# Kernel tuning notes

Hardware: AMD Instinct MI355X
Metric: run time of the kernel (lower is better)

Reference implementation:

```python
import jax, jax.numpy as jnp
import numpy as np

UPDATE_STEPS = 2
EPS = 1e-7


def _collect(attn, source, W, b):
    """_Collection_Unit: relu(Linear(source)) gathered by attention, row-averaged.
    attn: [N_tgt, N_src], source: [N_src, D_in], W: [D_out, D_in], b: [D_out]."""
    fc_out = jax.nn.relu(source @ W.T + b)          # [N_src, D_out]
    collect = attn @ fc_out                          # [N_tgt, D_out]
    denom = jnp.sum(attn, axis=1, keepdims=True) + EPS
    return collect / denom


def setup_inputs() -> dict:
    key = jax.random.key(0)
    ks = jax.random.split(key, 10)
    N_OBJ, N_REL, D = 2048, 16384, 1024
    inp = {
        "obj_feats": jax.random.normal(ks[0], (N_OBJ, D), jnp.float32),
        "rel_feats": jax.random.normal(ks[1], (N_REL, D), jnp.float32),
        "attn_sub": jax.random.uniform(ks[2], (N_OBJ, N_REL), jnp.float32),
        "attn_obj": jax.random.uniform(ks[3], (N_OBJ, N_REL), jnp.float32),
        "attn_self": jax.random.uniform(ks[4], (N_OBJ, N_OBJ), jnp.float32),
    }
    # normal_init(fc, 0, 0.01) per original module
    names = ["rel2obj_sub", "rel2obj_obj", "obj2rel_sub", "obj2rel_obj", "obj2obj"]
    for i, n in enumerate(names):
        inp[f"W_{n}"] = jax.random.normal(ks[5 + i], (D, D), jnp.float32) * 0.01
        inp[f"b_{n}"] = jnp.zeros((D,), jnp.float32)
    return inp


def reference(obj_feats, rel_feats, attn_sub, attn_obj, attn_self,
              W_rel2obj_sub, b_rel2obj_sub, W_rel2obj_obj, b_rel2obj_obj,
              W_obj2rel_sub, b_obj2rel_sub, W_obj2rel_obj, b_obj2rel_obj,
              W_obj2obj, b_obj2obj):
    x_obj, x_rel = obj_feats, rel_feats
    for _ in range(UPDATE_STEPS):
        # collect to objects: from relations (as subject / as object) and from other objects
        src_sub = _collect(attn_sub, x_rel, W_rel2obj_sub, b_rel2obj_sub)   # unit 0
        src_obj = _collect(attn_obj, x_rel, W_rel2obj_obj, b_rel2obj_obj)   # unit 1
        src_self = _collect(attn_self, x_obj, W_obj2obj, b_obj2obj)         # unit 4
        src2obj = (src_sub + src_obj + src_self) / 3.0
        x_obj_new = x_obj + src2obj                                          # _Update_Unit 0
        # collect to relations: from subject / object node features
        src_rel_sub = _collect(attn_sub.T, x_obj, W_obj2rel_sub, b_obj2rel_sub)  # unit 2
        src_rel_obj = _collect(attn_obj.T, x_obj, W_obj2rel_obj, b_obj2rel_obj)  # unit 3
        src2rel = (src_rel_sub + src_rel_obj) / 2.0
        x_rel = x_rel + src2rel                                              # _Update_Unit 1
        x_obj = x_obj_new
    return x_obj, x_rel
```

## Files before the change

kernel.cpp:

```cpp
#include <hip/hip_runtime.h>
#include <hip/hip_bf16.h>

typedef __attribute__((ext_vector_type(4))) float  f32x4;
typedef __attribute__((ext_vector_type(8))) __bf16 bf16x8;
typedef __attribute__((ext_vector_type(4))) int    i32x4;
typedef __attribute__((ext_vector_type(8))) int    i32x8;
typedef __hip_bfloat16 bf16_t;

#define GT 256
#define BM 128
#define BN 128
#define BK 32

#define NOBJ 2048
#define NREL 16384
#define DIM  1024
#define KOBJ 34816
#define KREL 4096

#define AS1Q __attribute__((address_space(1)))
#define AS3Q __attribute__((address_space(3)))

__device__ __forceinline__ void gload_lds16(const void* g, void* l) {
    __builtin_amdgcn_global_load_lds((AS1Q void*)const_cast<void*>(g),
                                     (AS3Q void*)l, 16, 0, 0);
}

#define MFMA_BF16 __builtin_amdgcn_mfma_f32_16x16x32_bf16
#define MFMA_F8(ACC, Af, Bf) \
    ACC = __builtin_amdgcn_mfma_scale_f32_16x16x128_f8f6f4( \
        Af, Bf, ACC, 0, 0, 0, 0x7F7F7F7F, 0, 0x7F7F7F7F)

#define VMCNT(N) asm volatile("s_waitcnt vmcnt(" #N ")" ::: "memory")
#define SBAR()   __builtin_amdgcn_sched_barrier(0)

__device__ __forceinline__ unsigned char fp8_byte(float x) {
    return (unsigned char)(__builtin_amdgcn_cvt_pk_fp8_f32(x, x, 0, false) & 0xFF);
}
__device__ __forceinline__ unsigned pk4_fp8(float a, float b, float c, float d) {
    int v = __builtin_amdgcn_cvt_pk_fp8_f32(a, b, 0, false);
    v = __builtin_amdgcn_cvt_pk_fp8_f32(c, d, v, true);
    return (unsigned)v;
}

__global__ __launch_bounds__(GT)
void gemm_bt_f234(const bf16_t* __restrict__ A, const bf16_t* __restrict__ B,
                  int M, int N, int K, const float* __restrict__ vecM,
                  unsigned char* __restrict__ fcRel8, unsigned char* __restrict__ fcObj8)
{
    __shared__ bf16_t sA[BM * BK];
    __shared__ bf16_t sB[BN * BK];

    const int tid  = threadIdx.x;
    const int lane = tid & 63;
    const int wid  = tid >> 6;
    const int wr = wid >> 1, wc = wid & 1;
    const int l15 = lane & 15, lk = lane >> 4;

    const long rowA0 = (long)blockIdx.x * BM;
    const long rowB0 = (long)blockIdx.y * BN;
    const long ldab  = (long)K * 2;

    const int c0 = tid, c1 = tid + GT;
    const int r0c = c0 >> 2, k0c = (c0 & 3) ^ ((r0c >> 1) & 3);
    const int r1c = c1 >> 2, k1c = (c1 & 3) ^ ((r1c >> 1) & 3);

    const char* gA0 = (const char*)A + (rowA0 + r0c) * ldab + k0c * 16;
    const char* gA1 = (const char*)A + (rowA0 + r1c) * ldab + k1c * 16;
    const char* gB0 = (const char*)B + (rowB0 + r0c) * ldab + k0c * 16;
    const char* gB1 = (const char*)B + (rowB0 + r1c) * ldab + k1c * 16;
    char* lA0 = (char*)sA + c0 * 16;
    char* lA1 = (char*)sA + c1 * 16;
    char* lB0 = (char*)sB + c0 * 16;
    char* lB1 = (char*)sB + c1 * 16;

    f32x4 acc[4][4];
    #pragma unroll
    for (int i = 0; i < 4; i++)
        #pragma unroll
        for (int j = 0; j < 4; j++) acc[i][j] = f32x4{0.f, 0.f, 0.f, 0.f};

    const int ktPer = K / BK;
    for (int kt = 0; kt < ktPer; ++kt) {
        const long kByte = (long)kt * (BK * 2);
        gload_lds16(gA0 + kByte, lA0);
        gload_lds16(gA1 + kByte, lA1);
        gload_lds16(gB0 + kByte, lB0);
        gload_lds16(gB1 + kByte, lB1);
        __syncthreads();

        bf16x8 af[4], bg[4];
        #pragma unroll
        for (int i = 0; i < 4; i++) {
            const int rr = wr * 64 + i * 16 + l15;
            const int kk = lk ^ ((rr >> 1) & 3);
            af[i] = *reinterpret_cast<const bf16x8*>((const char*)sA + rr * 64 + kk * 16);
        }
        #pragma unroll
        for (int j = 0; j < 4; j++) {
            const int rr = wc * 64 + j * 16 + l15;
            const int kk = lk ^ ((rr >> 1) & 3);
            bg[j] = *reinterpret_cast<const bf16x8*>((const char*)sB + rr * 64 + kk * 16);
        }
        #pragma unroll
        for (int i = 0; i < 4; i++)
            #pragma unroll
            for (int j = 0; j < 4; j++)
                acc[i][j] = MFMA_BF16(af[i], bg[j], acc[i][j], 0, 0, 0);
        __syncthreads();
    }

    #pragma unroll
    for (int i = 0; i < 4; i++) {
        const long mBase = rowA0 + wr * 64 + i * 16 + lk * 4;
        const f32x4 vm = *reinterpret_cast<const f32x4*>(&vecM[mBase]);
        #pragma unroll
        for (int r = 0; r < 4; r++) {
            const long m = mBase + r;
            #pragma unroll
            for (int j = 0; j < 4; j++) {
                const long n = rowB0 + wc * 64 + j * 16 + l15;
                const float v = fmaxf(acc[i][j][r] + vm[r], 0.f);
                const unsigned char o = fp8_byte(v);
                if (m < 1024)            fcRel8[m * (long)KREL + n] = o;
                else if (m < 2048)       fcRel8[(m - 1024) * (long)KREL + 2048 + n] = o;
                else                     fcObj8[(m - 2048) * (long)KOBJ + 32768 + n] = o;
            }
        }
    }
}

__global__ __launch_bounds__(512, 2)
void gemm256fc(const bf16_t* __restrict__ A, const bf16_t* __restrict__ B,
               int M, int N, int K, const float* __restrict__ vecM,
               unsigned char* __restrict__ Cb8, int ldc, int Ntiles)
{
    __shared__ __align__(16) char lds[131072];

    const int tid  = threadIdx.x;
    const int lane = tid & 63;
    const int wid  = tid >> 6;
    const int wr = wid >> 2, wc = wid & 3;
    const int l15 = lane & 15, lk = lane >> 4;

    const int nwg = gridDim.x;
    const int cpx = nwg >> 3;
    const int bid = blockIdx.x;
    const int swz = (bid & 7) * cpx + (bid >> 3);
    const int tm = swz / Ntiles, tn = swz % Ntiles;
    const long rowM0 = (long)tm * 256;
    const long rowN0 = (long)tn * 256;
    const long ld = (long)K * 2;

    const int NT = K >> 6;

    const int rl = tid >> 3;
    const int lc = (tid & 7) ^ (rl & 7);
    const char* gA0 = (const char*)A + (rowM0 + rl) * ld + lc * 16;
    const char* gB0 = (const char*)B + (rowN0 + rl) * ld + lc * 16;

    auto stage = [&](int buf, int isB, int h, int t) {
        const char* g = (isB ? gB0 : gA0) + (long)h * 128 * ld + (long)t * 128;
        char* l = (char*)lds + buf * 65536 + isB * 32768 + h * 16384 + tid * 16;
        gload_lds16(g, l);
        gload_lds16(g + 64 * ld, l + 8192);
    };

    const int xo0 = ((0 + lk) ^ (l15 & 7)) * 16;
    const int xo1 = ((4 + lk) ^ (l15 & 7)) * 16;
    const int baseA = (wr * 16 + l15) * 128;
    const int baseB = 32768 + (wc * 16 + l15) * 128;

    f32x4 acc[8][4];
    #pragma unroll
    for (int i = 0; i < 8; i++)
        #pragma unroll
        for (int j = 0; j < 4; j++) acc[i][j] = f32x4{0.f, 0.f, 0.f, 0.f};

    stage(0, 0, 0, 0); stage(0, 1, 0, 0); stage(0, 1, 1, 0); stage(0, 0, 1, 0);

    bf16x8 a[4][2], b[4][2];
    for (int t = 0; t < NT; ++t) {
        const int cur = t & 1;
        const int nxt = cur ^ 1;
        const bool pf = (t + 1) < NT;
        const char* lcur = (const char*)lds + (cur << 16);

        if (pf) { stage(nxt, 0, 0, t + 1); stage(nxt, 1, 0, t + 1);
                  stage(nxt, 1, 1, t + 1); stage(nxt, 0, 1, t + 1); }
        if (pf) { VMCNT(10); } else { VMCNT(2); }
        SBAR();
        __builtin_amdgcn_s_barrier();

        #pragma unroll
        for (int kf = 0; kf < 4; kf++) {
            a[kf][0] = *(const bf16x8*)(lcur + baseA + kf * 4096 + xo0);
            a[kf][1] = *(const bf16x8*)(lcur + baseA + kf * 4096 + xo1);
        }
        #pragma unroll
        for (int j = 0; j < 4; j++) {
            b[j][0] = *(const bf16x8*)(lcur + baseB + j * 8192 + xo0);
            b[j][1] = *(const bf16x8*)(lcur + baseB + j * 8192 + xo1);
        }
        asm volatile("s_waitcnt lgkmcnt(0)" ::: "memory");
        SBAR();
        __builtin_amdgcn_s_setprio(1);
        #pragma unroll
        for (int j = 0; j < 4; j++)
            #pragma unroll
            for (int kf = 0; kf < 4; kf++) {
                acc[kf][j] = MFMA_BF16(a[kf][0], b[j][0], acc[kf][j], 0, 0, 0);
                acc[kf][j] = MFMA_BF16(a[kf][1], b[j][1], acc[kf][j], 0, 0, 0);
            }
        __builtin_amdgcn_s_setprio(0);
        if (pf) { VMCNT(8); } else { VMCNT(0); }
        SBAR();
        __builtin_amdgcn_s_barrier();

        #pragma unroll
        for (int kf = 0; kf < 4; kf++) {
            a[kf][0] = *(const bf16x8*)(lcur + baseA + (4 + kf) * 4096 + xo0);
            a[kf][1] = *(const bf16x8*)(lcur + baseA + (4 + kf) * 4096 + xo1);
        }
        asm volatile("s_waitcnt lgkmcnt(0)" ::: "memory");
        SBAR();
        __builtin_amdgcn_s_barrier();
        __builtin_amdgcn_s_setprio(1);
        #pragma unroll
        for (int j = 0; j < 4; j++)
            #pragma unroll
            for (int kf = 0; kf < 4; kf++) {
                acc[4 + kf][j] = MFMA_BF16(a[kf][0], b[j][0], acc[4 + kf][j], 0, 0, 0);
                acc[4 + kf][j] = MFMA_BF16(a[kf][1], b[j][1], acc[4 + kf][j], 0, 0, 0);
            }
        __builtin_amdgcn_s_setprio(0);
    }

    #pragma unroll
    for (int kf = 0; kf < 8; kf++) {
        const long m0 = rowM0 + wr * 16 + kf * 32 + lk * 4;
        const f32x4 vm = *reinterpret_cast<const f32x4*>(vecM + m0);
        #pragma unroll
        for (int r = 0; r < 4; r++) {
            const long m = m0 + r;
            #pragma unroll
            for (int j = 0; j < 4; j++) {
                const long n = rowN0 + wc * 16 + j * 64 + l15;
                const float o = fmaxf(acc[kf][j][r] + vm[r], 0.f);
                Cb8[(m & 1023) * (long)ldc + (m >> 10) * 16384 + n] = fp8_byte(o);
            }
        }
    }
}

__global__ __launch_bounds__(512, 2)
void gemm256f8(const unsigned char* __restrict__ A, const unsigned char* __restrict__ B,
               int M, int N, int K, float* __restrict__ Cf, float scale,
               int ldc, int Ntiles)
{
    __shared__ __align__(16) char lds[131072];

    const int tid  = threadIdx.x;
    const int lane = tid & 63;
    const int wid  = tid >> 6;
    const int wr = wid >> 2, wc = wid & 3;
    const int l15 = lane & 15, lk = lane >> 4;

    const int nwg = gridDim.x;
    const int cpx = nwg >> 3;
    const int bid = blockIdx.x;
    const int swz = (bid & 7) * cpx + (bid >> 3);
    const int tm = swz / Ntiles, tn = swz % Ntiles;
    const long rowM0 = (long)tm * 256;
    const long rowN0 = (long)tn * 256;
    const long ld = (long)K;

    const int nz = gridDim.z;
    const int NT = (K >> 7) / nz;
    const long kb0 = (long)NT * blockIdx.z * 128;

    const int rl = tid >> 3;
    const int lc = (tid & 7) ^ (rl & 7);
    const char* gA0 = (const char*)A + (rowM0 + rl) * ld + kb0 + lc * 16;
    const char* gB0 = (const char*)B + (rowN0 + rl) * ld + kb0 + lc * 16;

    auto stage = [&](int buf, int isB, int h, int t) {
        const char* g = (isB ? gB0 : gA0) + (long)h * 128 * ld + (long)t * 128;
        char* l = (char*)lds + buf * 65536 + isB * 32768 + h * 16384 + tid * 16;
        gload_lds16(g, l);
        gload_lds16(g + 64 * ld, l + 8192);
    };

    const int xc0 = ((2 * lk + 0) ^ (l15 & 7)) * 16;
    const int xc1 = ((2 * lk + 1) ^ (l15 & 7)) * 16;
    const int baseA = (wr * 16 + l15) * 128;
    const int baseB = 32768 + (wc * 16 + l15) * 128;

#define LDF8(dst, off) { \
    i32x4 lo_ = *(const i32x4*)(lcur + (off) + xc0); \
    i32x4 hi_ = *(const i32x4*)(lcur + (off) + xc1); \
    dst = __builtin_shufflevector(lo_, hi_, 0, 1, 2, 3, 4, 5, 6, 7); }

    f32x4 acc[8][4];
    #pragma unroll
    for (int i = 0; i < 8; i++)
        #pragma unroll
        for (int j = 0; j < 4; j++) acc[i][j] = f32x4{0.f, 0.f, 0.f, 0.f};

    stage(0, 0, 0, 0); stage(0, 1, 0, 0); stage(0, 1, 1, 0); stage(0, 0, 1, 0);

    i32x8 a[4], b[4];
    for (int t = 0; t < NT; ++t) {
        const int cur = t & 1;
        const int nxt = cur ^ 1;
        const bool pf = (t + 1) < NT;
        const char* lcur = (const char*)lds + (cur << 16);

        if (pf) { stage(nxt, 0, 0, t + 1); stage(nxt, 1, 0, t + 1);
                  stage(nxt, 1, 1, t + 1); stage(nxt, 0, 1, t + 1); }
        if (pf) { VMCNT(10); } else { VMCNT(2); }
        SBAR();
        __builtin_amdgcn_s_barrier();

        #pragma unroll
        for (int kf = 0; kf < 4; kf++) LDF8(a[kf], baseA + kf * 4096);
        #pragma unroll
        for (int j = 0; j < 4; j++)    LDF8(b[j], baseB + j * 8192);
        asm volatile("s_waitcnt lgkmcnt(0)" ::: "memory");
        SBAR();
        __builtin_amdgcn_s_setprio(1);
        #pragma unroll
        for (int j = 0; j < 4; j++)
            #pragma unroll
            for (int kf = 0; kf < 4; kf++) MFMA_F8(acc[kf][j], a[kf], b[j]);
        __builtin_amdgcn_s_setprio(0);
        if (pf) { VMCNT(8); } else { VMCNT(0); }
        SBAR();
        __builtin_amdgcn_s_barrier();

        #pragma unroll
        for (int kf = 0; kf < 4; kf++) LDF8(a[kf], baseA + (4 + kf) * 4096);
        asm volatile("s_waitcnt lgkmcnt(0)" ::: "memory");
        SBAR();
        __builtin_amdgcn_s_barrier();
        __builtin_amdgcn_s_setprio(1);
        #pragma unroll
        for (int j = 0; j < 4; j++)
            #pragma unroll
            for (int kf = 0; kf < 4; kf++) MFMA_F8(acc[4 + kf][j], a[kf], b[j]);
        __builtin_amdgcn_s_setprio(0);
    }
#undef LDF8

    #pragma unroll
    for (int kf = 0; kf < 8; kf++) {
        const long m0 = rowM0 + wr * 16 + kf * 32 + lk * 4;
        #pragma unroll
        for (int r = 0; r < 4; r++) {
            const long m = m0 + r;
            #pragma unroll
            for (int j = 0; j < 4; j++) {
                const long n = rowN0 + wc * 16 + j * 64 + l15;
                const float v = acc[kf][j][r] * scale;
                if (nz == 1) Cf[m * (long)ldc + n] += v;
                else atomicAdd(&Cf[m * (long)ldc + n], v);
            }
        }
    }
}

__global__ __launch_bounds__(256)
void k_cast_bf16(const float* __restrict__ in, bf16_t* __restrict__ out, long n)
{
    const long stride = (long)gridDim.x * blockDim.x;
    for (long i = (long)blockIdx.x * blockDim.x + threadIdx.x; i * 4 < n; i += stride) {
        f32x4 v = *reinterpret_cast<const f32x4*>(in + i * 4);
        union { bf16_t h[4]; ushort4 u; } o;
        o.h[0] = __float2bfloat16(v[0]); o.h[1] = __float2bfloat16(v[1]);
        o.h[2] = __float2bfloat16(v[2]); o.h[3] = __float2bfloat16(v[3]);
        *reinterpret_cast<ushort4*>(out + i * 4) = o.u;
    }
}

template<bool COLS>
__global__ __launch_bounds__(256)
void k_sums(const float* __restrict__ in, int C,
            float* __restrict__ rowsum, float* __restrict__ colsum)
{
    __shared__ float cpart[16][64];
    __shared__ float rpart[64][17];
    const int tid = threadIdx.x;
    const int tx  = tid & 15;
    const int ty  = tid >> 4;
    const long c0 = (long)blockIdx.x * 64;
    const long r0 = (long)blockIdx.y * 64;

    float cs0 = 0.f, cs1 = 0.f, cs2 = 0.f, cs3 = 0.f;
    #pragma unroll
    for (int i = 0; i < 4; i++) {
        const int r = i * 16 + ty;
        const f32x4 v = *reinterpret_cast<const f32x4*>(&in[(r0 + r) * (long)C + c0 + tx * 4]);
        rpart[r][tx] = v[0] + v[1] + v[2] + v[3];
        cs0 += v[0]; cs1 += v[1]; cs2 += v[2]; cs3 += v[3];
    }
    if (COLS) {
        cpart[ty][tx * 4 + 0] = cs0;
        cpart[ty][tx * 4 + 1] = cs1;
        cpart[ty][tx * 4 + 2] = cs2;
        cpart[ty][tx * 4 + 3] = cs3;
    }
    __syncthreads();
    if (tid < 64) {
        float rs = 0.f;
        #pragma unroll
        for (int k = 0; k < 16; k++) rs += rpart[tid][k];
        atomicAdd(&rowsum[r0 + tid], rs);
        if (COLS) {
            float cs = 0.f;
            #pragma unroll
            for (int k = 0; k < 16; k++) cs += cpart[k][tid];
            atomicAdd(&colsum[c0 + tid], cs);
        }
    }
}

__global__ __launch_bounds__(256)
void k_invscale(float* __restrict__ s, int n, float c)
{
    const int i = blockIdx.x * 256 + threadIdx.x;
    if (i < n) s[i] = c / (s[i] + 1e-7f);
}

template<bool TRANS>
__global__ __launch_bounds__(256)
void k_prep2f8(const float* __restrict__ in, int C,
               unsigned char* __restrict__ Aobj, unsigned char* __restrict__ Arel,
               const float* __restrict__ invRow, const float* __restrict__ invCol)
{
    __shared__ float tile[64][65];
    const int tid = threadIdx.x;
    const int tx  = tid & 15;
    const int ty  = tid >> 4;
    const long c0 = (long)blockIdx.x * 64;
    const long r0 = (long)blockIdx.y * 64;

    #pragma unroll
    for (int i = 0; i < 4; i++) {
        const int r = i * 16 + ty;
        const f32x4 v = *reinterpret_cast<const f32x4*>(&in[(r0 + r) * (long)C + c0 + tx * 4]);
        const float sc = invRow[r0 + r];
        *reinterpret_cast<unsigned*>(&Aobj[(r0 + r) * (long)KOBJ + c0 + tx * 4]) =
            pk4_fp8(v[0] * sc, v[1] * sc, v[2] * sc, v[3] * sc);
        if (TRANS) *reinterpret_cast<f32x4*>(&tile[r][tx * 4]) = v;
    }
    if (TRANS) {
        __syncthreads();
        const int rr = tid & 63;
        const int cg = tid >> 6;
        #pragma unroll
        for (int i = 0; i < 16; i++) {
            const int c = cg * 16 + i;
            const float sc = invCol[c0 + c];
            Arel[(c0 + c) * (long)KREL + r0 + rr] = fp8_byte(tile[rr][c] * sc);
        }
    }
}

extern "C" void kernel_launch(void* const* d_in, const int* in_sizes, int n_in,
                              void* d_out, int out_size, void* d_ws, size_t ws_size,
                              hipStream_t stream)
{
    if (n_in < 15) return;
    const float* obj_feats = (const float*)d_in[0];
    const float* rel_feats = (const float*)d_in[1];
    const float* attn_sub  = (const float*)d_in[2];
    const float* attn_obj  = (const float*)d_in[3];
    const float* attn_self = (const float*)d_in[4];
    const float* Wf[5] = { (const float*)d_in[5], (const float*)d_in[7],
                           (const float*)d_in[9], (const float*)d_in[11], (const float*)d_in[13] };
    const float* Bf[5] = { (const float*)d_in[6], (const float*)d_in[8],
                           (const float*)d_in[10], (const float*)d_in[12], (const float*)d_in[14] };

    const int NO = NOBJ, NR = NREL, D = DIM;

    char* w = (char*)d_ws;
    auto take = [&](size_t bytes) { char* p = w; w += bytes; return p; };
    unsigned char* Aobj8  = (unsigned char*)take((size_t)NO * KOBJ);
    unsigned char* Arel8  = (unsigned char*)take((size_t)NR * KREL);
    unsigned char* fcObj8 = (unsigned char*)take((size_t)D * KOBJ);
    unsigned char* fcRel8 = (unsigned char*)take((size_t)D * KREL);
    bf16_t* xrel_bf = (bf16_t*)take((size_t)NR * D * 2);
    bf16_t* xobj_bf = (bf16_t*)take((size_t)NO * D * 2);
    bf16_t* Wstk01  = (bf16_t*)take((size_t)2 * D * D * 2);
    bf16_t* Wstk234 = (bf16_t*)take((size_t)3 * D * D * 2);
    float*  b01     = (float*)take((size_t)2 * D * 4);
    float*  bstk    = (float*)take((size_t)3 * D * 4);
    float*  sums    = (float*)take((size_t)(3 * NO + 2 * NR) * 4);
    float* invS     = sums;
    float* invO     = sums + NO;
    float* invSelf  = sums + 2 * NO;
    float* invTS    = sums + 3 * NO;
    float* invTO    = sums + 3 * NO + NR;
    if ((size_t)(w - (char*)d_ws) > ws_size) return;

    float* x_obj = (float*)d_out;
    float* x_rel = x_obj + (size_t)NO * D;

    hipMemcpyAsync(x_obj, obj_feats, (size_t)NO * D * 4, hipMemcpyDeviceToDevice, stream);
    hipMemcpyAsync(x_rel, rel_feats, (size_t)NR * D * 4, hipMemcpyDeviceToDevice, stream);
    hipMemcpyAsync(b01,     Bf[0], (size_t)D * 4, hipMemcpyDeviceToDevice, stream);
    hipMemcpyAsync(b01 + D, Bf[1], (size_t)D * 4, hipMemcpyDeviceToDevice, stream);
    for (int i = 0; i < 3; i++)
        hipMemcpyAsync(bstk + i * D, Bf[2 + i], (size_t)D * 4, hipMemcpyDeviceToDevice, stream);
    hipMemsetAsync(sums, 0, (size_t)(3 * NO + 2 * NR) * 4, stream);

    auto cast = [&](const float* in, bf16_t* out, long n) {
        long blocks = (n / 4 + 255) / 256; if (blocks > 4096) blocks = 4096;
        k_cast_bf16<<<dim3((unsigned)blocks), dim3(256), 0, stream>>>(in, out, n);
    };
    cast(Wf[0], Wstk01,                 (long)D * D);
    cast(Wf[1], Wstk01 + (size_t)D * D, (long)D * D);
    for (int i = 0; i < 3; i++)
        cast(Wf[2 + i], Wstk234 + (size_t)i * D * D, (long)D * D);

    k_sums<true><<<dim3(NR / 64, NO / 64), dim3(256), 0, stream>>>(attn_sub, NR, invS, invTS);
    k_sums<true><<<dim3(NR / 64, NO / 64), dim3(256), 0, stream>>>(attn_obj, NR, invO, invTO);
    k_sums<false><<<dim3(NO / 64, NO / 64), dim3(256), 0, stream>>>(attn_self, NO, invSelf, nullptr);
    k_invscale<<<dim3((3 * NO + 255) / 256), dim3(256), 0, stream>>>(sums, 3 * NO, 8192.f / 3.f);
    k_invscale<<<dim3((2 * NR + 255) / 256), dim3(256), 0, stream>>>(sums + 3 * NO, 2 * NR, 1024.f);

    k_prep2f8<true><<<dim3(NR / 64, NO / 64), dim3(256), 0, stream>>>(
        attn_sub, NR, Aobj8, Arel8, invS, invTS);
    k_prep2f8<true><<<dim3(NR / 64, NO / 64), dim3(256), 0, stream>>>(
        attn_obj, NR, Aobj8 + 16384, Arel8 + 2048, invO, invTO);
    k_prep2f8<false><<<dim3(NO / 64, NO / 64), dim3(256), 0, stream>>>(
        attn_self, NO, Aobj8 + 32768, nullptr, invSelf, nullptr);

    for (int step = 0; step < 2; ++step) {
        cast(x_obj, xobj_bf, (long)NO * D);
        cast(x_rel, xrel_bf, (long)NR * D);

        gemm256fc<<<dim3((2 * D / 256) * (NR / 256), 1, 1), dim3(512), 0, stream>>>(
            Wstk01, xrel_bf, 2 * D, NR, D, b01, fcObj8, KOBJ, NR / 256);
        gemm_bt_f234<<<dim3(3 * D / BM, NO / BN, 1), dim3(GT), 0, stream>>>(
            Wstk234, xobj_bf, 3 * D, NO, D, bstk, fcRel8, fcObj8);

        gemm256f8<<<dim3((NO / 256) * (D / 256), 1, 8), dim3(512), 0, stream>>>(
            Aobj8, fcObj8, NO, D, KOBJ, x_obj, 1.f / 8192.f, D, D / 256);
        gemm256f8<<<dim3((NR / 256) * (D / 256), 1, 1), dim3(512), 0, stream>>>(
            Arel8, fcRel8, NR, D, KREL, x_rel, 1.f / 2048.f, D, D / 256);
    }
}
```

Before: 961.6 us.

## Replace double-buffered 256x256 FP8 GEMM with single-buffered 128x256 high-occupancy variant

Replaces the 256x256 double-buffered FP8 attention GEMM with a 128x256 tile kernel that uses 48KB of LDS, one buffer, and half the accumulators. Launch bounds rise to 4 blocks per CU, so more waves can hide latency and the grid doubles. Software prefetch is dropped in favour of plain __syncthreads loads each k-step, which exposes global load latency within each block and lowers reuse of the B operand per tile.

```diff
diff --git a/kernel.cpp b/kernel.cpp
--- a/kernel.cpp
+++ b/kernel.cpp
@@ -253,12 +253,12 @@
     }
 }
 
-__global__ __launch_bounds__(512, 2)
-void gemm256f8(const unsigned char* __restrict__ A, const unsigned char* __restrict__ B,
-               int M, int N, int K, float* __restrict__ Cf, float scale,
-               int ldc, int Ntiles)
-{
-    __shared__ __align__(16) char lds[131072];
+__global__ __launch_bounds__(512, 4)
+void gemmf8_occ(const unsigned char* __restrict__ A, const unsigned char* __restrict__ B,
+                int M, int N, int K, float* __restrict__ Cf, float scale,
+                int ldc, int Ntiles)
+{
+    __shared__ __align__(16) char lds[49152];
 
     const int tid  = threadIdx.x;
     const int lane = tid & 63;
@@ -271,7 +271,7 @@
     const int bid = blockIdx.x;
     const int swz = (bid & 7) * cpx + (bid >> 3);
     const int tm = swz / Ntiles, tn = swz % Ntiles;
-    const long rowM0 = (long)tm * 256;
+    const long rowM0 = (long)tm * 128;
     const long rowN0 = (long)tn * 256;
     const long ld = (long)K;
 
@@ -279,88 +279,61 @@
     const int NT = (K >> 7) / nz;
     const long kb0 = (long)NT * blockIdx.z * 128;
 
-    const int rl = tid >> 3;
-    const int lc = (tid & 7) ^ (rl & 7);
-    const char* gA0 = (const char*)A + (rowM0 + rl) * ld + kb0 + lc * 16;
-    const char* gB0 = (const char*)B + (rowN0 + rl) * ld + kb0 + lc * 16;
-
-    auto stage = [&](int buf, int isB, int h, int t) {
-        const char* g = (isB ? gB0 : gA0) + (long)h * 128 * ld + (long)t * 128;
-        char* l = (char*)lds + buf * 65536 + isB * 32768 + h * 16384 + tid * 16;
-        gload_lds16(g, l);
-        gload_lds16(g + 64 * ld, l + 8192);
-    };
+    const int rs = tid >> 3;
+    const int kc = (tid & 7) ^ (rs & 7);
+    const char* gA = (const char*)A + (rowM0 + rs) * ld + kb0 + kc * 16;
+    const char* gB = (const char*)B + (rowN0 + rs) * ld + kb0 + kc * 16;
+    char* lA = (char*)lds + tid * 16;
+    char* lB = (char*)lds + 16384 + tid * 16;
 
     const int xc0 = ((2 * lk + 0) ^ (l15 & 7)) * 16;
     const int xc1 = ((2 * lk + 1) ^ (l15 & 7)) * 16;
-    const int baseA = (wr * 16 + l15) * 128;
-    const int baseB = 32768 + (wc * 16 + l15) * 128;
+    const int baseA = (wr * 64 + l15) * 128;
+    const int baseB = 16384 + (wc * 64 + l15) * 128;
 
 #define LDF8(dst, off) { \
-    i32x4 lo_ = *(const i32x4*)(lcur + (off) + xc0); \
-    i32x4 hi_ = *(const i32x4*)(lcur + (off) + xc1); \
+    i32x4 lo_ = *(const i32x4*)((const char*)lds + (off) + xc0); \
+    i32x4 hi_ = *(const i32x4*)((const char*)lds + (off) + xc1); \
     dst = __builtin_shufflevector(lo_, hi_, 0, 1, 2, 3, 4, 5, 6, 7); }
 
-    f32x4 acc[8][4];
-    #pragma unroll
-    for (int i = 0; i < 8; i++)
+    f32x4 acc[4][4];
+    #pragma unroll
+    for (int i = 0; i < 4; i++)
         #pragma unroll
         for (int j = 0; j < 4; j++) acc[i][j] = f32x4{0.f, 0.f, 0.f, 0.f};
 
-    stage(0, 0, 0, 0); stage(0, 1, 0, 0); stage(0, 1, 1, 0); stage(0, 0, 1, 0);
-
-    i32x8 a[4], b[4];
     for (int t = 0; t < NT; ++t) {
-        const int cur = t & 1;
-        const int nxt = cur ^ 1;
-        const bool pf = (t + 1) < NT;
-        const char* lcur = (const char*)lds + (cur << 16);
-
-        if (pf) { stage(nxt, 0, 0, t + 1); stage(nxt, 1, 0, t + 1);
-                  stage(nxt, 1, 1, t + 1); stage(nxt, 0, 1, t + 1); }
-        if (pf) { VMCNT(10); } else { VMCNT(2); }
-        SBAR();
-        __builtin_amdgcn_s_barrier();
-
-        #pragma unroll
-        for (int kf = 0; kf < 4; kf++) LDF8(a[kf], baseA + kf * 4096);
-        #pragma unroll
-        for (int j = 0; j < 4; j++)    LDF8(b[j], baseB + j * 8192);
-        asm volatile("s_waitcnt lgkmcnt(0)" ::: "memory");
-        SBAR();
-        __builtin_amdgcn_s_setprio(1);
-        #pragma unroll
-        for (int j = 0; j < 4; j++)
-            #pragma unroll
-            for (int kf = 0; kf < 4; kf++) MFMA_F8(acc[kf][j], a[kf], b[j]);
-        __builtin_amdgcn_s_setprio(0);
-        if (pf) { VMCNT(8); } else { VMCNT(0); }
-        SBAR();
-        __builtin_amdgcn_s_barrier();
-
-        #pragma unroll
-        for (int kf = 0; kf < 4; kf++) LDF8(a[kf], baseA + (4 + kf) * 4096);
-        asm volatile("s_waitcnt lgkmcnt(0)" ::: "memory");
-        SBAR();
-        __builtin_amdgcn_s_barrier();
-        __builtin_amdgcn_s_setprio(1);
-        #pragma unroll
-        for (int j = 0; j < 4; j++)
-            #pragma unroll
-            for (int kf = 0; kf < 4; kf++) MFMA_F8(acc[4 + kf][j], a[kf], b[j]);
-        __builtin_amdgcn_s_setprio(0);
+        const long kByte = (long)t * 128;
+        gload_lds16(gA + kByte, lA);
+        gload_lds16(gA + kByte + 64 * ld, lA + 8192);
+        #pragma unroll
+        for (int i = 0; i < 4; i++)
+            gload_lds16(gB + kByte + (long)i * 64 * ld, lB + i * 8192);
+        __syncthreads();
+
+        i32x8 a[4];
+        #pragma unroll
+        for (int kf = 0; kf < 4; kf++) LDF8(a[kf], baseA + kf * 2048);
+        #pragma unroll
+        for (int j = 0; j < 4; j++) {
+            i32x8 b;
+            LDF8(b, baseB + j * 2048);
+            #pragma unroll
+            for (int kf = 0; kf < 4; kf++) MFMA_F8(acc[kf][j], a[kf], b);
+        }
+        __syncthreads();
     }
 #undef LDF8
 
     #pragma unroll
-    for (int kf = 0; kf < 8; kf++) {
-        const long m0 = rowM0 + wr * 16 + kf * 32 + lk * 4;
+    for (int kf = 0; kf < 4; kf++) {
+        const long m0 = rowM0 + wr * 64 + kf * 16 + lk * 4;
         #pragma unroll
         for (int r = 0; r < 4; r++) {
             const long m = m0 + r;
             #pragma unroll
             for (int j = 0; j < 4; j++) {
-                const long n = rowN0 + wc * 16 + j * 64 + l15;
+                const long n = rowN0 + wc * 64 + j * 16 + l15;
                 const float v = acc[kf][j][r] * scale;
                 if (nz == 1) Cf[m * (long)ldc + n] += v;
                 else atomicAdd(&Cf[m * (long)ldc + n], v);
@@ -545,9 +518,9 @@
         gemm_bt_f234<<<dim3(3 * D / BM, NO / BN, 1), dim3(GT), 0, stream>>>(
             Wstk234, xobj_bf, 3 * D, NO, D, bstk, fcRel8, fcObj8);
 
-        gemm256f8<<<dim3((NO / 256) * (D / 256), 1, 8), dim3(512), 0, stream>>>(
+        gemmf8_occ<<<dim3((NO / 128) * (D / 256), 1, 8), dim3(512), 0, stream>>>(
             Aobj8, fcObj8, NO, D, KOBJ, x_obj, 1.f / 8192.f, D, D / 256);
-        gemm256f8<<<dim3((NR / 256) * (D / 256), 1, 1), dim3(512), 0, stream>>>(
+        gemmf8_occ<<<dim3((NR / 128) * (D / 256), 1, 1), dim3(512), 0, stream>>>(
             Arel8, fcRel8, NR, D, KREL, x_rel, 1.f / 2048.f, D, D / 256);
     }
 }
```

New measurement: 897.9 us. -6.6%, faster.
